# Optimization experiments

Hardware: AMD Instinct MI355X
Metric: run time of the kernel (lower is better)

The kernel has to match this reference:

```python
import jax, jax.numpy as jnp
import numpy as np

DIM = 4096

def _fwht_unnormalized(y):
    # y: (T, d), iterative radix-2 butterfly, unnormalized Sylvester WHT
    d = y.shape[-1]
    h = 1
    while h < d:
        y = y.reshape(-1, d // (2 * h), 2, h)
        a = y[..., 0, :]
        b = y[..., 1, :]
        y = jnp.stack([a + b, a - b], axis=-2).reshape(-1, d)
        h *= 2
    return y

def setup_inputs() -> dict:
    key = jax.random.key(0)
    x = jax.random.normal(key, (4, 2048, DIM), dtype=jnp.float32)
    return {"x": x}

def reference(x):
    # Original: x_flat @ H.T where H is built recursively with a 1/sqrt(n)
    # division at EVERY recursion level. H is symmetric, and equals the
    # unnormalized Sylvester Hadamard times 2^{-L(L+1)/4}, L = log2(d).
    shape = x.shape
    d = shape[-1]
    L = int(round(np.log2(d)))
    scale = np.float32(2.0 ** (-(L * (L + 1)) / 4.0))
    y = _fwht_unnormalized(x.reshape(-1, d))
    return (y * scale).reshape(shape)
```

## Files before the change

### kernel.cpp

```cpp
#include <hip/hip_runtime.h>


constexpr int DIM = 4096;
constexpr int PITCH = 17;
constexpr int NBLOCKS = 2048;

__device__ __forceinline__ void fwht16(float v[16]) {
#pragma unroll
    for (int h = 1; h < 16; h <<= 1) {
#pragma unroll
        for (int i = 0; i < 16; i += 2 * h) {
#pragma unroll
            for (int k = 0; k < h; ++k) {
                float a = v[i + k];
                float b = v[i + k + h];
                v[i + k]     = a + b;
                v[i + k + h] = a - b;
            }
        }
    }
}

__global__ __launch_bounds__(256, 8) void fwht4096_kernel(const float* __restrict__ x,
                                                          float* __restrict__ y,
                                                          int nrows) {
    __shared__ float buf[PITCH * 256];
    const int t = threadIdx.x;
    const int t_hi = t >> 4;
    const int t_lo = t & 15;

    float4 nxt[4];
    long long row = blockIdx.x;
    if (row < nrows) {
        const float4* src = reinterpret_cast<const float4*>(x + row * DIM + t * 16);
#pragma unroll
        for (int q = 0; q < 4; ++q) nxt[q] = src[q];
    }

    for (; row < nrows; row += NBLOCKS) {
        float v[16];
#pragma unroll
        for (int q = 0; q < 4; ++q) {
            v[4 * q + 0] = nxt[q].x;
            v[4 * q + 1] = nxt[q].y;
            v[4 * q + 2] = nxt[q].z;
            v[4 * q + 3] = nxt[q].w;
        }

        fwht16(v);

        __syncthreads();

        {
            float* wp = buf + PITCH * t;
#pragma unroll
            for (int j = 0; j < 16; ++j) wp[j] = v[j];
        }
        __syncthreads();
        {
            const float* rp = buf + (PITCH * 16) * t_hi + t_lo;
#pragma unroll
            for (int j = 0; j < 16; ++j) v[j] = rp[PITCH * j];
        }

        fwht16(v);

        {
            const long long nrow = row + NBLOCKS;
            if (nrow < nrows) {
                const float4* src =
                    reinterpret_cast<const float4*>(x + nrow * DIM + t * 16);
#pragma unroll
                for (int q = 0; q < 4; ++q) nxt[q] = src[q];
            }
        }

        __syncthreads();

        {
            float* wp = buf + PITCH * t_lo + t_hi;
#pragma unroll
            for (int j = 0; j < 16; ++j) wp[(PITCH * 16) * j] = v[j];
        }
        __syncthreads();
        {
            const float* rp = buf + PITCH * t;
#pragma unroll
            for (int j = 0; j < 16; ++j) v[j] = rp[j];
        }

        fwht16(v);

        const float scale = 0x1p-39f;
        float* dst = y + row * DIM + t;
#pragma unroll
        for (int j = 0; j < 16; ++j) {
            __builtin_nontemporal_store(v[j] * scale, dst + j * 256);
        }
    }
}

extern "C" void kernel_launch(void* const* d_in, const int* in_sizes, int n_in,
                              void* d_out, int out_size, void* d_ws, size_t ws_size,
                              hipStream_t stream) {
    const float* x = (const float*)d_in[0];
    float* y = (float*)d_out;
    const int nrows = in_sizes[0] / DIM;
    const int grid = nrows < NBLOCKS ? nrows : NBLOCKS;
    fwht4096_kernel<<<grid, 256, 0, stream>>>(x, y, nrows);
}
```

Measured before the change: 231.1 us.

## Prefetch rows into LDS via async global_load_lds and trim block barriers

Replaces the register-based prefetch of the next row with async global-to-LDS loads (global_load_lds) into a per-wave swizzled staging buffer. Each wave waits on vmcnt/lgkmcnt counters instead of using full __syncthreads, so only two block barriers remain around the cross-wave transpose. The grid is halved to 1024 persistent blocks and the launch-bounds occupancy hint drops to 4. This is meant to hide global load latency and cut barrier stalls, at the cost of extra LDS per block and fragile hand-written waitcnt ordering.

```diff
diff --git a/kernel.cpp b/kernel.cpp
--- a/kernel.cpp
+++ b/kernel.cpp
@@ -3,7 +3,7 @@
 
 constexpr int DIM = 4096;
 constexpr int PITCH = 17;
-constexpr int NBLOCKS = 2048;
+constexpr int NBLOCKS = 1024;
 
 __device__ __forceinline__ void fwht16(float v[16]) {
 #pragma unroll
@@ -21,70 +21,86 @@
     }
 }
 
-__global__ __launch_bounds__(256, 8) void fwht4096_kernel(const float* __restrict__ x,
+__device__ __forceinline__ void stage_quarter(const float* gsrc_base, float* lds_base) {
+#pragma unroll
+    for (int i = 0; i < 4; ++i) {
+        __builtin_amdgcn_global_load_lds(
+            (const __attribute__((address_space(1))) float*)(gsrc_base + i * 256),
+            (__attribute__((address_space(3))) float*)(lds_base + i * 256), 16, 0, 0);
+    }
+}
+
+__global__ __launch_bounds__(256, 4) void fwht4096_kernel(const float* __restrict__ x,
                                                           float* __restrict__ y,
                                                           int nrows) {
-    __shared__ float buf[PITCH * 256];
+    __shared__ __align__(16) float stage[DIM];
+    __shared__ float tbuf[PITCH * 256];
     const int t = threadIdx.x;
+    const int w = t >> 6;
+    const int l = t & 63;
     const int t_hi = t >> 4;
     const int t_lo = t & 15;
+    const int swz = l ^ ((l >> 2) & 7) ^ ((l >> 4) & 1);
 
-    float4 nxt[4];
+    float* my_stage = stage + w * 1024;
+    const int g_off = w * 1024 + swz * 4;
+
     long long row = blockIdx.x;
-    if (row < nrows) {
-        const float4* src = reinterpret_cast<const float4*>(x + row * DIM + t * 16);
-#pragma unroll
-        for (int q = 0; q < 4; ++q) nxt[q] = src[q];
-    }
+    stage_quarter(x + row * DIM + g_off, my_stage);
+    asm volatile("s_waitcnt vmcnt(0)" ::: "memory");
 
     for (; row < nrows; row += NBLOCKS) {
+        asm volatile("s_waitcnt vmcnt(16)" ::: "memory");
+        __builtin_amdgcn_sched_barrier(0);
+
         float v[16];
 #pragma unroll
         for (int q = 0; q < 4; ++q) {
-            v[4 * q + 0] = nxt[q].x;
-            v[4 * q + 1] = nxt[q].y;
-            v[4 * q + 2] = nxt[q].z;
-            v[4 * q + 3] = nxt[q].w;
+            const int chunk = (4 * t + q) ^ (t & 7);
+            float4 d = *reinterpret_cast<const float4*>(stage + 4 * chunk);
+            v[4 * q + 0] = d.x;
+            v[4 * q + 1] = d.y;
+            v[4 * q + 2] = d.z;
+            v[4 * q + 3] = d.w;
         }
 
         fwht16(v);
 
-        __syncthreads();
+        asm volatile("s_waitcnt lgkmcnt(0)" ::: "memory");
+        __builtin_amdgcn_sched_barrier(0);
+        {
+            const long long nrow = row + NBLOCKS;
+            if (nrow < nrows) stage_quarter(x + nrow * DIM + g_off, my_stage);
+        }
+        __builtin_amdgcn_sched_barrier(0);
 
         {
-            float* wp = buf + PITCH * t;
+            float* wp = tbuf + PITCH * t;
 #pragma unroll
             for (int j = 0; j < 16; ++j) wp[j] = v[j];
         }
-        __syncthreads();
         {
-            const float* rp = buf + (PITCH * 16) * t_hi + t_lo;
+            const float* rp = tbuf + (PITCH * 16) * t_hi + t_lo;
 #pragma unroll
             for (int j = 0; j < 16; ++j) v[j] = rp[PITCH * j];
         }
 
         fwht16(v);
 
-        {
-            const long long nrow = row + NBLOCKS;
-            if (nrow < nrows) {
-                const float4* src =
-                    reinterpret_cast<const float4*>(x + nrow * DIM + t * 16);
-#pragma unroll
-                for (int q = 0; q < 4; ++q) nxt[q] = src[q];
-            }
-        }
-
-        __syncthreads();
+        asm volatile("" ::: "memory");
+        __builtin_amdgcn_s_barrier();
+        asm volatile("" ::: "memory");
 
         {
-            float* wp = buf + PITCH * t_lo + t_hi;
+            float* wp = tbuf + PITCH * t_lo + t_hi;
 #pragma unroll
             for (int j = 0; j < 16; ++j) wp[(PITCH * 16) * j] = v[j];
         }
-        __syncthreads();
+        asm volatile("s_waitcnt lgkmcnt(0)" ::: "memory");
+        __builtin_amdgcn_s_barrier();
+        asm volatile("" ::: "memory");
         {
-            const float* rp = buf + PITCH * t;
+            const float* rp = tbuf + PITCH * t;
 #pragma unroll
             for (int j = 0; j < 16; ++j) v[j] = rp[j];
         }
```

Measured after the change: 231.0 us. About the same (-0.0%).
